# Kernel optimization log

Measured on AMD Instinct MI355X. Metric: run time of the kernel, lower is better.

The kernel has to match this reference:

```python
import jax, jax.numpy as jnp
import numpy as np

SEQ, D_IN, D_H, D_OUT = 8192, 1024, 2048, 1024


def setup_inputs() -> dict:
    key = jax.random.key(0)
    ks = jax.random.split(key, 5)
    # small init scales keep tanh out of full saturation (torch code uses randn,
    # but unit-scale weights would saturate; math is identical regardless of scale)
    return {
        "x_seq": jax.random.normal(ks[0], (SEQ, D_IN), jnp.float32),
        "h0": jnp.zeros((D_H,), jnp.float32),
        "W_ih": jax.random.normal(ks[1], (D_H, D_IN), jnp.float32) / np.sqrt(D_IN),
        "W_hh": jax.random.normal(ks[2], (D_H, D_H), jnp.float32) / np.sqrt(D_H),
        "b_h": jnp.zeros((D_H,), jnp.float32),
        "W_ho_w": jax.random.normal(ks[3], (D_OUT, D_H), jnp.float32) / np.sqrt(D_H),
        "W_ho_b": jnp.zeros((D_OUT,), jnp.float32),
    }


def reference(x_seq, h0, W_ih, W_hh, b_h, W_ho_w, W_ho_b):
    # Precompute the input projection for all steps at once (same math as
    # W_ih @ x_t per step, just batched): (S, H)
    xw = x_seq @ W_ih.T + b_h

    def step(h, xw_t):
        h = jnp.tanh(xw_t + W_hh @ h)  # recurrent matvec + tanh
        return h, h

    h_final, hs = jax.lax.scan(step, h0, xw)  # hs: (S, H)
    outputs = hs @ W_ho_w.T + W_ho_b          # (S, O)
    return outputs, h_final
```

## Files before the change

### kernel.cpp

```cpp
#include <hip/hip_runtime.h>
#include <hip/hip_bf16.h>

#define SEQ   8192
#define DIN   1024
#define DH    2048
#define DOUT  1024

#define SENT 0x7fc0deadu

__global__ __launch_bounds__(256) void fill_sent_kernel(uint4* __restrict__ p, size_t n4) {
    size_t i = (size_t)blockIdx.x * blockDim.x + threadIdx.x;
    size_t stride = (size_t)gridDim.x * blockDim.x;
    uint4 v = make_uint4(SENT, SENT, SENT, SENT);
    for (; i < n4; i += stride) p[i] = v;
}

__global__ __launch_bounds__(256) void gemm_nt_bias(
    const float* __restrict__ A, const float* __restrict__ B,
    const float* __restrict__ bias, float* __restrict__ C,
    int M, int N, int K) {
    __shared__ float As[16][132];
    __shared__ float Bs[16][68];
    const int tid = threadIdx.x;
    const int bm = blockIdx.x * 128;
    const int bn = blockIdx.y * 64;
    const int alr = tid >> 1;
    const int alk = (tid & 1) * 8;
    const int blr = tid >> 2;
    const int blk = (tid & 3) * 4;
    const int tm = (tid >> 4) * 8;
    const int tn = (tid & 15) * 4;
    float acc[8][4] = {};

    for (int k0 = 0; k0 < K; k0 += 16) {
        const float4 a0 = *(const float4*)&A[(size_t)(bm + alr) * K + k0 + alk];
        const float4 a1 = *(const float4*)&A[(size_t)(bm + alr) * K + k0 + alk + 4];
        const float4 bv = *(const float4*)&B[(size_t)(bn + blr) * K + k0 + blk];
        As[alk + 0][alr] = a0.x; As[alk + 1][alr] = a0.y;
        As[alk + 2][alr] = a0.z; As[alk + 3][alr] = a0.w;
        As[alk + 4][alr] = a1.x; As[alk + 5][alr] = a1.y;
        As[alk + 6][alr] = a1.z; As[alk + 7][alr] = a1.w;
        Bs[blk + 0][blr] = bv.x; Bs[blk + 1][blr] = bv.y;
        Bs[blk + 2][blr] = bv.z; Bs[blk + 3][blr] = bv.w;
        __syncthreads();
#pragma unroll
        for (int k = 0; k < 16; ++k) {
            const float4 af0 = *(const float4*)&As[k][tm];
            const float4 af1 = *(const float4*)&As[k][tm + 4];
            const float4 bf  = *(const float4*)&Bs[k][tn];
            const float a[8] = {af0.x, af0.y, af0.z, af0.w,
                                af1.x, af1.y, af1.z, af1.w};
            const float b[4] = {bf.x, bf.y, bf.z, bf.w};
#pragma unroll
            for (int i = 0; i < 8; ++i)
#pragma unroll
                for (int j = 0; j < 4; ++j)
                    acc[i][j] = fmaf(a[i], b[j], acc[i][j]);
        }
        __syncthreads();
    }

    const float4 bv = *(const float4*)&bias[bn + tn];
#pragma unroll
    for (int i = 0; i < 8; ++i) {
        float4 o;
        o.x = acc[i][0] + bv.x;
        o.y = acc[i][1] + bv.y;
        o.z = acc[i][2] + bv.z;
        o.w = acc[i][3] + bv.w;
        *(float4*)&C[(size_t)(bm + tm + i) * N + bn + tn] = o;
    }
}

__global__ __attribute__((amdgpu_flat_work_group_size(512, 512),
                          amdgpu_waves_per_eu(2, 2)))
void rnn_recurrence(
    const float* __restrict__ Whh, const float* __restrict__ xw,
    const float* __restrict__ h0, float* __restrict__ hs) {
    __shared__ float h_lds[2][DH];
    __shared__ float h_out[16];
    const int tid = threadIdx.x;
    const int wave = tid >> 6;
    const int lane = tid & 63;
    const int row0 = blockIdx.x * 16 + wave * 2;

    float4 w4[2][8];
#pragma unroll
    for (int r = 0; r < 2; ++r)
#pragma unroll
        for (int j = 0; j < 8; ++j) {
            w4[r][j] = *(const float4*)&Whh[(size_t)(row0 + r) * DH + lane * 4 + 256 * j];
            asm volatile("" : "+v"(w4[r][j].x), "+v"(w4[r][j].y),
                              "+v"(w4[r][j].z), "+v"(w4[r][j].w));
        }

    for (int t = 0; t < SEQ; ++t) {
        const int par = t & 1;
        const float xwv = xw[(size_t)t * DH + row0 + (lane & 1)];

        if (t == 0) {
            *(float4*)&h_lds[0][4 * tid] = *(const float4*)&h0[4 * tid];
        } else {
            const float* src = hs + (size_t)(t - 1) * DH;
            const float* a0 = src + 4 * tid;
            float4 va;
            unsigned bad;
            do {
                asm volatile(
                    "global_load_dwordx4 %0, %1, off sc0 sc1\n\t"
                    "s_waitcnt vmcnt(0)"
                    : "=&v"(va)
                    : "v"(a0)
                    : "memory");
                bad = (__float_as_uint(va.x) == SENT) | (__float_as_uint(va.y) == SENT) |
                      (__float_as_uint(va.z) == SENT) | (__float_as_uint(va.w) == SENT);
            } while (__builtin_expect(bad != 0, 0));
            *(float4*)&h_lds[par][4 * tid] = va;
        }
        __syncthreads();

        float4 h4[8];
#pragma unroll
        for (int j = 0; j < 8; ++j)
            h4[j] = *(const float4*)&h_lds[par][lane * 4 + 256 * j];

        float acc0 = 0.f, acc1 = 0.f;
#pragma unroll
        for (int j = 0; j < 8; ++j) {
            const float4 hv = h4[j];
            acc0 = fmaf(w4[0][j].x, hv.x, acc0); acc0 = fmaf(w4[0][j].y, hv.y, acc0);
            acc0 = fmaf(w4[0][j].z, hv.z, acc0); acc0 = fmaf(w4[0][j].w, hv.w, acc0);
            acc1 = fmaf(w4[1][j].x, hv.x, acc1); acc1 = fmaf(w4[1][j].y, hv.y, acc1);
            acc1 = fmaf(w4[1][j].z, hv.z, acc1); acc1 = fmaf(w4[1][j].w, hv.w, acc1);
        }

        float p = (lane & 1) ? acc1 : acc0;
        float q = (lane & 1) ? acc0 : acc1;
        p += __shfl_xor(q, 1);
        p += __shfl_xor(p, 2);
        p += __shfl_xor(p, 4);
        p += __shfl_xor(p, 8);
        p += __shfl_xor(p, 16);
        p += __shfl_xor(p, 32);

        if (lane < 2)
            h_out[wave * 2 + lane] = tanhf(p + xwv);
        __syncthreads();
        if (tid < 16)
            __hip_atomic_store((unsigned*)(hs + (size_t)t * DH + blockIdx.x * 16 + tid),
                               __float_as_uint(h_out[tid]),
                               __ATOMIC_RELAXED, __HIP_MEMORY_SCOPE_AGENT);
    }
}

__global__ __launch_bounds__(256) void copy_hfinal(const float* __restrict__ hs,
                                                   float* __restrict__ out) {
    const int i = blockIdx.x * 256 + threadIdx.x;
    out[i] = hs[(size_t)(SEQ - 1) * DH + i];
}

extern "C" void kernel_launch(void* const* d_in, const int* in_sizes, int n_in,
                              void* d_out, int out_size, void* d_ws, size_t ws_size,
                              hipStream_t stream) {
    (void)in_sizes; (void)n_in; (void)out_size; (void)ws_size;
    const float* x_seq  = (const float*)d_in[0];
    const float* h0     = (const float*)d_in[1];
    const float* W_ih   = (const float*)d_in[2];
    const float* W_hh   = (const float*)d_in[3];
    const float* b_h    = (const float*)d_in[4];
    const float* W_ho_w = (const float*)d_in[5];
    const float* W_ho_b = (const float*)d_in[6];
    float* out = (float*)d_out;

    float* xw = (float*)d_ws;
    float* hs = xw + (size_t)SEQ * DH;

    fill_sent_kernel<<<2048, 256, 0, stream>>>((uint4*)hs, (size_t)SEQ * DH / 4);

    gemm_nt_bias<<<dim3(SEQ / 128, DH / 64), 256, 0, stream>>>(
        x_seq, W_ih, b_h, xw, SEQ, DH, DIN);

    rnn_recurrence<<<DH / 16, 512, 0, stream>>>(W_hh, xw, h0, hs);

    gemm_nt_bias<<<dim3(SEQ / 128, DOUT / 64), 256, 0, stream>>>(
        hs, W_ho_w, W_ho_b, out, SEQ, DOUT, DH);

    copy_hfinal<<<DH / 256, 256, 0, stream>>>(hs, out + (size_t)SEQ * DOUT);
}
```

Baseline: 15.00 ms.

## Split recurrent matvec by columns per thread, dropping LDS broadcast of h

Each thread now holds one 4-column slice of all 16 rows of W_hh, so the h vector it polls from global memory is used straight from registers. The h_lds staging, the LDS reload and one of the two block barriers per step are gone. A transpose-style butterfly shuffle reduces the 16 row partials within each wave, and a small LDS array then sums the 8 waves' partials before tanh and the store. This is meant to cut per-step latency on the serial recurrence chain. The cost is more shuffle instructions, plus a cross-wave sum done serially by 16 threads.

```diff
diff --git a/kernel.cpp b/kernel.cpp
--- a/kernel.cpp
+++ b/kernel.cpp
@@ -77,79 +77,93 @@
 void rnn_recurrence(
     const float* __restrict__ Whh, const float* __restrict__ xw,
     const float* __restrict__ h0, float* __restrict__ hs) {
-    __shared__ float h_lds[2][DH];
-    __shared__ float h_out[16];
+    __shared__ float part[2][8][16];
     const int tid = threadIdx.x;
     const int wave = tid >> 6;
     const int lane = tid & 63;
-    const int row0 = blockIdx.x * 16 + wave * 2;
-
-    float4 w4[2][8];
-#pragma unroll
-    for (int r = 0; r < 2; ++r)
-#pragma unroll
-        for (int j = 0; j < 8; ++j) {
-            w4[r][j] = *(const float4*)&Whh[(size_t)(row0 + r) * DH + lane * 4 + 256 * j];
-            asm volatile("" : "+v"(w4[r][j].x), "+v"(w4[r][j].y),
-                              "+v"(w4[r][j].z), "+v"(w4[r][j].w));
-        }
+    const int rbase = blockIdx.x * 16;
+    const int c0 = 4 * tid;
+
+    float4 w[16];
+#pragma unroll
+    for (int r = 0; r < 16; ++r) {
+        w[r] = *(const float4*)&Whh[(size_t)(rbase + r) * DH + c0];
+        asm volatile("" : "+v"(w[r].x), "+v"(w[r].y), "+v"(w[r].z), "+v"(w[r].w));
+    }
 
     for (int t = 0; t < SEQ; ++t) {
         const int par = t & 1;
-        const float xwv = xw[(size_t)t * DH + row0 + (lane & 1)];
-
+        float xwv = 0.f;
+        if (tid < 16) xwv = xw[(size_t)t * DH + rbase + tid];
+
+        float4 hv;
         if (t == 0) {
-            *(float4*)&h_lds[0][4 * tid] = *(const float4*)&h0[4 * tid];
+            hv = *(const float4*)&h0[c0];
         } else {
-            const float* src = hs + (size_t)(t - 1) * DH;
-            const float* a0 = src + 4 * tid;
-            float4 va;
+            const float* a0 = hs + (size_t)(t - 1) * DH + c0;
             unsigned bad;
             do {
                 asm volatile(
                     "global_load_dwordx4 %0, %1, off sc0 sc1\n\t"
                     "s_waitcnt vmcnt(0)"
-                    : "=&v"(va)
-                    : "v"(a0)
-                    : "memory");
-                bad = (__float_as_uint(va.x) == SENT) | (__float_as_uint(va.y) == SENT) |
-                      (__float_as_uint(va.z) == SENT) | (__float_as_uint(va.w) == SENT);
+                    : "=&v"(hv) : "v"(a0) : "memory");
+                bad = (__float_as_uint(hv.x) == SENT) | (__float_as_uint(hv.y) == SENT) |
+                      (__float_as_uint(hv.z) == SENT) | (__float_as_uint(hv.w) == SENT);
             } while (__builtin_expect(bad != 0, 0));
-            *(float4*)&h_lds[par][4 * tid] = va;
-        }
+        }
+
+        float acc[16];
+#pragma unroll
+        for (int r = 0; r < 16; ++r)
+            acc[r] = fmaf(w[r].w, hv.w,
+                     fmaf(w[r].z, hv.z,
+                     fmaf(w[r].y, hv.y, w[r].x * hv.x)));
+
+        const bool b0 = (lane & 1) != 0, b1 = (lane & 2) != 0,
+                   b2 = (lane & 4) != 0, b3 = (lane & 8) != 0;
+        float s8[8];
+#pragma unroll
+        for (int j = 0; j < 8; ++j) {
+            const float k = b0 ? acc[2 * j + 1] : acc[2 * j];
+            const float g = b0 ? acc[2 * j]     : acc[2 * j + 1];
+            s8[j] = k + __shfl_xor(g, 1);
+        }
+        float s4[4];
+#pragma unroll
+        for (int j = 0; j < 4; ++j) {
+            const float k = b1 ? s8[2 * j + 1] : s8[2 * j];
+            const float g = b1 ? s8[2 * j]     : s8[2 * j + 1];
+            s4[j] = k + __shfl_xor(g, 2);
+        }
+        float s2[2];
+#pragma unroll
+        for (int j = 0; j < 2; ++j) {
+            const float k = b2 ? s4[2 * j + 1] : s4[2 * j];
+            const float g = b2 ? s4[2 * j]     : s4[2 * j + 1];
+            s2[j] = k + __shfl_xor(g, 4);
+        }
+        float s1;
+        {
+            const float k = b3 ? s2[1] : s2[0];
+            const float g = b3 ? s2[0] : s2[1];
+            s1 = k + __shfl_xor(g, 8);
+        }
+        s1 += __shfl_xor(s1, 16);
+        s1 += __shfl_xor(s1, 32);
+
+        if (lane < 16) part[par][wave][lane] = s1;
         __syncthreads();
 
-        float4 h4[8];
-#pragma unroll
-        for (int j = 0; j < 8; ++j)
-            h4[j] = *(const float4*)&h_lds[par][lane * 4 + 256 * j];
-
-        float acc0 = 0.f, acc1 = 0.f;
-#pragma unroll
-        for (int j = 0; j < 8; ++j) {
-            const float4 hv = h4[j];
-            acc0 = fmaf(w4[0][j].x, hv.x, acc0); acc0 = fmaf(w4[0][j].y, hv.y, acc0);
-            acc0 = fmaf(w4[0][j].z, hv.z, acc0); acc0 = fmaf(w4[0][j].w, hv.w, acc0);
-            acc1 = fmaf(w4[1][j].x, hv.x, acc1); acc1 = fmaf(w4[1][j].y, hv.y, acc1);
-            acc1 = fmaf(w4[1][j].z, hv.z, acc1); acc1 = fmaf(w4[1][j].w, hv.w, acc1);
-        }
-
-        float p = (lane & 1) ? acc1 : acc0;
-        float q = (lane & 1) ? acc0 : acc1;
-        p += __shfl_xor(q, 1);
-        p += __shfl_xor(p, 2);
-        p += __shfl_xor(p, 4);
-        p += __shfl_xor(p, 8);
-        p += __shfl_xor(p, 16);
-        p += __shfl_xor(p, 32);
-
-        if (lane < 2)
-            h_out[wave * 2 + lane] = tanhf(p + xwv);
-        __syncthreads();
-        if (tid < 16)
-            __hip_atomic_store((unsigned*)(hs + (size_t)t * DH + blockIdx.x * 16 + tid),
-                               __float_as_uint(h_out[tid]),
+        if (tid < 16) {
+            const float sum =
+                part[par][0][tid] + part[par][1][tid] + part[par][2][tid] +
+                part[par][3][tid] + part[par][4][tid] + part[par][5][tid] +
+                part[par][6][tid] + part[par][7][tid];
+            const float hval = tanhf(sum + xwv);
+            __hip_atomic_store((unsigned*)(hs + (size_t)t * DH + rbase + tid),
+                               __float_as_uint(hval),
                                __ATOMIC_RELAXED, __HIP_MEMORY_SCOPE_AGENT);
+        }
     }
 }
 
```

New measurement: 14.57 ms. -2.9%, faster.
